# Kernel tuning notes

Measured on AMD Instinct MI355X. Metric: run time of the kernel, lower is better.

## Reference

```python
import jax, jax.numpy as jnp
import numpy as np

# Module/problem constants (match init_kwargs & input_specs)
B, D, H, W = 2, 96, 96, 96
CIN, COUT, K = 16, 32, 3
N = 200000  # number of active (sparse) voxels


def setup_inputs() -> dict:
    key = jax.random.key(0)
    kf, kw, kb = jax.random.split(key, 3)
    # unique valid voxel coordinates -> deterministic scatter semantics
    rng = np.random.default_rng(0)
    lin = rng.choice(B * D * H * W, size=N, replace=False)
    b, z, y, x = np.unravel_index(lin, (B, D, H, W))
    indices = jnp.asarray(np.stack([b, z, y, x], axis=1).astype(np.int32))  # [N,4]
    features = jax.random.normal(kf, (N, CIN), dtype=jnp.float32)
    fan_in = CIN * K ** 3
    conv_w = jax.random.normal(kw, (COUT, CIN, K, K, K), dtype=jnp.float32) / np.sqrt(fan_in)
    conv_b = jax.random.normal(kb, (COUT,), dtype=jnp.float32) * 0.01
    return {"features": features, "indices": indices, "conv_w": conv_w, "conv_b": conv_b}


def reference(features, indices, conv_w, conv_b):
    """DenseFallbackConv3d.forward on a SparseConvTensor, stride=1 path.

    1) scatter sparse features into dense grid [B,CIN,D,H,W]
    2) dense Conv3d (k=3, pad=1, stride=1) + bias
    3) gather per-point output features at the same voxel indices -> [N,COUT]
    """
    b = indices[:, 0]
    z = indices[:, 1]
    y = indices[:, 2]
    x = indices[:, 3]
    # scatter: equivalent of grid[b, :, z, y, x] = features
    grid = jnp.zeros((B, CIN, D, H, W), dtype=features.dtype).at[b, :, z, y, x].set(features)
    out = jax.lax.conv_general_dilated(
        grid, conv_w,
        window_strides=(1, 1, 1),
        padding=((1, 1), (1, 1), (1, 1)),
        dimension_numbers=("NCDHW", "OIDHW", "NCDHW"),
    )
    out = out + conv_b[None, :, None, None, None]
    # gather: out_dense[b, :, z, y, x] for every active voxel -> [N, COUT]
    return out[b, :, z, y, x]
```

## Files before the change

### kernel.cpp

```cpp
#include <hip/hip_runtime.h>

#define BB   2
#define DD   96
#define HH   96
#define WW   96
#define CINC 16
#define COUTC 32
#define KVOL 27
#define GRID_VOX (BB*DD*HH*WW)
#define NW (KVOL*CINC*COUTC)
#define VPT 8
#define CVB (256*VPT)
#define SWP 20

typedef _Float16 half4 __attribute__((ext_vector_type(4)));
typedef _Float16 half8 __attribute__((ext_vector_type(8)));
typedef float    floatx16 __attribute__((ext_vector_type(16)));

__global__ __launch_bounds__(256) void setup_kernel(
        const int* __restrict__ idx, int* __restrict__ g,
        const float* __restrict__ w, _Float16* __restrict__ wH,
        int* __restrict__ counter, int n, int scatter_blocks) {
    if ((int)blockIdx.x < scatter_blocks) {
        int i = blockIdx.x * 256 + threadIdx.x;
        if (i >= n) return;
        int4 v = ((const int4*)idx)[i];
        int lin = ((v.x * DD + v.y) * HH + v.z) * WW + v.w;
        g[lin] = i;
    } else {
        int t = ((int)blockIdx.x - scatter_blocks) * 256 + threadIdx.x;
        if (t == 0) counter[0] = 0;
        if (t >= NW) return;
        int ci = t & (CINC - 1);
        int co = (t >> 4) & (COUTC - 1);
        int kk = t >> 9;
        wH[t] = (_Float16)w[(co * CINC + ci) * KVOL + kk];
    }
}

__global__ __launch_bounds__(256) void compact_kernel(
        const int* __restrict__ idx, const float* __restrict__ feat,
        int* __restrict__ g, _Float16* __restrict__ featH,
        int* __restrict__ pc, int* __restrict__ perm,
        int* __restrict__ counter, int n) {
    __shared__ int s_wsum[4];
    __shared__ int s_wbase[4];
    __shared__ int s_base;
    const int t = threadIdx.x;
    const int lane = t & 63;
    const int wv = t >> 6;
    const int base = blockIdx.x * CVB + t * VPT;

    int4 a0 = ((const int4*)(g + base))[0];
    int4 a1 = ((const int4*)(g + base))[1];
    int vals[VPT] = {a0.x, a0.y, a0.z, a0.w, a1.x, a1.y, a1.z, a1.w};
    int pid[VPT], pck[VPT];
    int cnt = 0;
#pragma unroll
    for (int q = 0; q < VPT; ++q) {
        int p = vals[q];
        bool ok = ((unsigned)p < (unsigned)n);
        int pk = 0;
        if (ok) {
            int4 c = ((const int4*)idx)[p];
            int lin = ((c.x * DD + c.y) * HH + c.z) * WW + c.w;
            ok = (lin == base + q);
            pk = (c.x << 21) | (c.y << 14) | (c.z << 7) | c.w;
        }
        pid[q] = ok ? p : -1;
        pck[q] = pk;
        cnt += ok ? 1 : 0;
    }

    int incl = cnt;
#pragma unroll
    for (int d = 1; d < 64; d <<= 1) {
        int v = __shfl_up(incl, d);
        if (lane >= d) incl += v;
    }
    if (lane == 63) s_wsum[wv] = incl;
    __syncthreads();
    if (t == 0) {
        int t0 = s_wsum[0], t1 = s_wsum[1], t2 = s_wsum[2], t3 = s_wsum[3];
        s_wbase[0] = 0; s_wbase[1] = t0; s_wbase[2] = t0 + t1;
        s_wbase[3] = t0 + t1 + t2;
        s_base = atomicAdd(counter, t0 + t1 + t2 + t3);
    }
    __syncthreads();
    int o = s_base + s_wbase[wv] + incl - cnt;

#pragma unroll
    for (int q = 0; q < VPT; ++q) {
        int tag = n;
        int p = pid[q];
        if (p >= 0) {
            pc[o] = pck[q];
            perm[o] = p;
            const float4* src = (const float4*)(feat + (size_t)p * CINC);
            float4 f0 = src[0], f1 = src[1], f2 = src[2], f3 = src[3];
            half8 h0, h1;
            h0[0]=(_Float16)f0.x; h0[1]=(_Float16)f0.y; h0[2]=(_Float16)f0.z; h0[3]=(_Float16)f0.w;
            h0[4]=(_Float16)f1.x; h0[5]=(_Float16)f1.y; h0[6]=(_Float16)f1.z; h0[7]=(_Float16)f1.w;
            h1[0]=(_Float16)f2.x; h1[1]=(_Float16)f2.y; h1[2]=(_Float16)f2.z; h1[3]=(_Float16)f2.w;
            h1[4]=(_Float16)f3.x; h1[5]=(_Float16)f3.y; h1[6]=(_Float16)f3.z; h1[7]=(_Float16)f3.w;
            half8* dst = (half8*)(featH + (size_t)o * CINC);
            dst[0] = h0; dst[1] = h1;
            tag = o;
            ++o;
        }
        g[base + q] = tag;
    }
    if (blockIdx.x == 0 && t == 0) {
        half8* zr = (half8*)(featH + (size_t)n * CINC);
        half8 hz = {};
        zr[0] = hz; zr[1] = hz;
    }
}

__global__ __launch_bounds__(256, 4) void conv_mfma_kernel(
        const _Float16* __restrict__ featH, const int* __restrict__ pc,
        const int* __restrict__ perm, const _Float16* __restrict__ wH,
        const float* __restrict__ bias, const int* __restrict__ g,
        float* __restrict__ out, int n) {
    __shared__ _Float16 sW[KVOL * 32 * SWP];
    const int lane = threadIdx.x & 63;
    const int wave = threadIdx.x >> 6;
    const int m    = lane & 31;
    const int hf   = lane >> 5;

    for (int u = threadIdx.x; u < KVOL * 64; u += 256) {
        int kk = u >> 6, r = u & 63;
        int co = r >> 1, h = r & 1;
        const half4* src = (const half4*)(wH + kk * (COUTC * CINC) + co * CINC + h * 8);
        half4 v0 = src[0], v1 = src[1];
        _Float16* dst = &sW[kk * 32 * SWP + co * SWP + h * 8];
        *(half4*)dst = v0;
        *(half4*)(dst + 4) = v1;
    }
    __syncthreads();

    const int j0 = (blockIdx.x * 4 + wave) * 32;
    if (j0 >= n) return;
    const int j = j0 + m;

    const int p = pc[j];
    const int x = p & 127, y = (p >> 7) & 127, z = (p >> 14) & 127, b = p >> 21;
    const int base = ((b * DD + z) * HH + y) * WW + x;
    const int pm = perm[j];

    int nid[KVOL];
#pragma unroll
    for (int kk = 0; kk < KVOL; ++kk) {
        const int dz = kk / 9 - 1, dy = (kk / 3) % 3 - 1, dx = kk % 3 - 1;
        int nz = z + dz, ny = y + dy, nx = x + dx;
        bool inb = ((unsigned)nz < DD) & ((unsigned)ny < HH) & ((unsigned)nx < WW);
        int addr = inb ? base + (dz * HH + dy) * WW + dx : 0;
        int v = g[addr];
        nid[kk] = inb ? v : n;
    }

    float bval = bias[m];
    floatx16 acc0, acc1;
#pragma unroll
    for (int i = 0; i < 16; ++i) { acc0[i] = bval; acc1[i] = 0.0f; }

#pragma unroll
    for (int gq = 0; gq < 3; ++gq) {
        half8 av[9];
#pragma unroll
        for (int q = 0; q < 9; ++q)
            av[q] = *(const half8*)(featH + (size_t)nid[gq * 9 + q] * CINC + hf * 8);
#pragma unroll
        for (int q = 0; q < 9; ++q) {
            const int kk = gq * 9 + q;
            const _Float16* bp = &sW[kk * 32 * SWP + m * SWP + hf * 8];
            half4 b0 = *(const half4*)bp;
            half4 b1 = *(const half4*)(bp + 4);
            half8 bf;
            bf[0]=b0[0]; bf[1]=b0[1]; bf[2]=b0[2]; bf[3]=b0[3];
            bf[4]=b1[0]; bf[5]=b1[1]; bf[6]=b1[2]; bf[7]=b1[3];
            if (kk & 1)
                acc1 = __builtin_amdgcn_mfma_f32_32x32x16_f16(av[q], bf, acc1, 0, 0, 0);
            else
                acc0 = __builtin_amdgcn_mfma_f32_32x32x16_f16(av[q], bf, acc0, 0, 0, 0);
        }
    }

#pragma unroll
    for (int i = 0; i < 16; ++i) {
        int r = (i & 3) + 8 * (i >> 2) + 4 * hf;
        int row = __shfl(pm, r);
        out[(size_t)row * COUTC + m] = acc0[i] + acc1[i];
    }
}

extern "C" void kernel_launch(void* const* d_in, const int* in_sizes, int n_in,
                              void* d_out, int out_size, void* d_ws, size_t ws_size,
                              hipStream_t stream) {
    const float* feat  = (const float*)d_in[0];
    const int*   idx   = (const int*)d_in[1];
    const float* convw = (const float*)d_in[2];
    const float* convb = (const float*)d_in[3];
    float* out = (float*)d_out;

    const int n = in_sizes[1] / 4;

    char* ws = (char*)d_ws;
    int*      g       = (int*)ws;
    int*      counter = (int*)(ws + GRID_VOX * 4);
    int*      pc      = (int*)(ws + GRID_VOX * 4 + 256);
    int*      perm    = pc + n;
    _Float16* featH   = (_Float16*)(perm + n);
    _Float16* wH      = featH + (size_t)(n + 1) * CINC;

    const int sb = (n + 255) / 256;
    const int rb = (NW + 255) / 256;
    setup_kernel<<<sb + rb, 256, 0, stream>>>(idx, g, convw, wH, counter, n, sb);
    compact_kernel<<<GRID_VOX / CVB, 256, 0, stream>>>(
        idx, feat, g, featH, pc, perm, counter, n);

    const int waves = (n + 31) / 32;
    conv_mfma_kernel<<<(waves + 3) / 4, 256, 0, stream>>>(
        featH, pc, perm, wH, convb, g, out, n);
}
```

Before: 123.4 us.

## Fuse scatter, compaction and conv into one cooperative persistent kernel

Replaces the three kernel launches with a single cooperative kernel, sized to the occupancy-limited resident block count, that separates the scatter, compaction and MFMA convolution phases with grid-wide barriers. Weights are converted straight into shared memory per block, so the separate half-precision weight buffer is no longer built. The aim is to remove kernel launch gaps and tail effects between stages. In exchange it adds grid-sync cost, grid-stride loops with fewer blocks, and host-side occupancy queries on every call. The conv loop uses n>>5 tiles, which silently drops a trailing partial tile when n is not a multiple of 32 (here n is a multiple of 32).

```diff
diff --git a/kernel.cpp b/kernel.cpp
--- a/kernel.cpp
+++ b/kernel.cpp
@@ -1,4 +1,7 @@
 #include <hip/hip_runtime.h>
+#include <hip/hip_cooperative_groups.h>
+
+namespace cg = cooperative_groups;
 
 #define BB   2
 #define DD   96
@@ -11,11 +14,179 @@
 #define NW (KVOL*CINC*COUTC)
 #define VPT 8
 #define CVB (256*VPT)
+#define NCHUNK (GRID_VOX / CVB)
 #define SWP 20
 
 typedef _Float16 half4 __attribute__((ext_vector_type(4)));
 typedef _Float16 half8 __attribute__((ext_vector_type(8)));
 typedef float    floatx16 __attribute__((ext_vector_type(16)));
+
+__global__ __launch_bounds__(256, 4) void fused_kernel(
+        const float* __restrict__ feat, const int* __restrict__ idx,
+        const float* __restrict__ w, const float* __restrict__ bias,
+        int* __restrict__ g, _Float16* __restrict__ featH,
+        int* __restrict__ pc, int* __restrict__ perm,
+        int* __restrict__ counter, float* __restrict__ out, int n) {
+    __shared__ _Float16 sW[KVOL * 32 * SWP];
+    cg::grid_group grid = cg::this_grid();
+    const int t = threadIdx.x;
+    const int nblk = gridDim.x;
+
+    for (int u = t; u < KVOL * 64; u += 256) {
+        int kk = u >> 6, r = u & 63;
+        int co = r >> 1, h = r & 1;
+        half8 v;
+#pragma unroll
+        for (int q = 0; q < 8; ++q)
+            v[q] = (_Float16)w[(co * CINC + h * 8 + q) * KVOL + kk];
+        _Float16* dst = &sW[kk * 32 * SWP + co * SWP + h * 8];
+        *(half4*)dst = half4{v[0], v[1], v[2], v[3]};
+        *(half4*)(dst + 4) = half4{v[4], v[5], v[6], v[7]};
+    }
+
+    for (int i = blockIdx.x * 256 + t; i < n; i += nblk * 256) {
+        int4 v = ((const int4*)idx)[i];
+        int lin = ((v.x * DD + v.y) * HH + v.z) * WW + v.w;
+        g[lin] = i;
+    }
+    if (blockIdx.x == 0 && t == 0) {
+        counter[0] = 0;
+        half8 hz = {};
+        half8* zr = (half8*)(featH + (size_t)n * CINC);
+        zr[0] = hz; zr[1] = hz;
+    }
+    grid.sync();
+
+    {
+        __shared__ int s_wsum[4];
+        __shared__ int s_wbase[4];
+        __shared__ int s_base;
+        const int lane = t & 63;
+        const int wv = t >> 6;
+        for (int chunk = blockIdx.x; chunk < NCHUNK; chunk += nblk) {
+            const int base = chunk * CVB + t * VPT;
+
+            int4 a0 = ((const int4*)(g + base))[0];
+            int4 a1 = ((const int4*)(g + base))[1];
+            int vals[VPT] = {a0.x, a0.y, a0.z, a0.w, a1.x, a1.y, a1.z, a1.w};
+            int pid[VPT], pck[VPT];
+            int cnt = 0;
+#pragma unroll
+            for (int q = 0; q < VPT; ++q) {
+                int p = vals[q];
+                bool ok = ((unsigned)p < (unsigned)n);
+                int pk = 0;
+                if (ok) {
+                    int4 c = ((const int4*)idx)[p];
+                    int lin = ((c.x * DD + c.y) * HH + c.z) * WW + c.w;
+                    ok = (lin == base + q);
+                    pk = (c.x << 21) | (c.y << 14) | (c.z << 7) | c.w;
+                }
+                pid[q] = ok ? p : -1;
+                pck[q] = pk;
+                cnt += ok ? 1 : 0;
+            }
+
+            int incl = cnt;
+#pragma unroll
+            for (int d = 1; d < 64; d <<= 1) {
+                int v = __shfl_up(incl, d);
+                if (lane >= d) incl += v;
+            }
+            if (lane == 63) s_wsum[wv] = incl;
+            __syncthreads();
+            if (t == 0) {
+                int t0 = s_wsum[0], t1 = s_wsum[1], t2 = s_wsum[2], t3 = s_wsum[3];
+                s_wbase[0] = 0; s_wbase[1] = t0; s_wbase[2] = t0 + t1;
+                s_wbase[3] = t0 + t1 + t2;
+                s_base = atomicAdd(counter, t0 + t1 + t2 + t3);
+            }
+            __syncthreads();
+            int o = s_base + s_wbase[wv] + incl - cnt;
+
+#pragma unroll
+            for (int q = 0; q < VPT; ++q) {
+                int tag = n;
+                int p = pid[q];
+                if (p >= 0) {
+                    pc[o] = pck[q];
+                    perm[o] = p;
+                    const float4* src = (const float4*)(feat + (size_t)p * CINC);
+                    float4 f0 = src[0], f1 = src[1], f2 = src[2], f3 = src[3];
+                    half8 h0, h1;
+                    h0[0]=(_Float16)f0.x; h0[1]=(_Float16)f0.y; h0[2]=(_Float16)f0.z; h0[3]=(_Float16)f0.w;
+                    h0[4]=(_Float16)f1.x; h0[5]=(_Float16)f1.y; h0[6]=(_Float16)f1.z; h0[7]=(_Float16)f1.w;
+                    h1[0]=(_Float16)f2.x; h1[1]=(_Float16)f2.y; h1[2]=(_Float16)f2.z; h1[3]=(_Float16)f2.w;
+                    h1[4]=(_Float16)f3.x; h1[5]=(_Float16)f3.y; h1[6]=(_Float16)f3.z; h1[7]=(_Float16)f3.w;
+                    half8* dst = (half8*)(featH + (size_t)o * CINC);
+                    dst[0] = h0; dst[1] = h1;
+                    tag = o;
+                    ++o;
+                }
+                g[base + q] = tag;
+            }
+        }
+    }
+    grid.sync();
+
+    const int lane = t & 63;
+    const int wave = t >> 6;
+    const int m    = lane & 31;
+    const int hf   = lane >> 5;
+    const float bval = bias[m];
+    const int ntile = n >> 5;
+
+#pragma unroll 1
+    for (int tile = blockIdx.x * 4 + wave; tile < ntile; tile += nblk * 4) {
+        const int j = tile * 32 + m;
+        const int p = pc[j];
+        const int x = p & 127, y = (p >> 7) & 127, z = (p >> 14) & 127, b = p >> 21;
+        const int base = ((b * DD + z) * HH + y) * WW + x;
+        const int pm = perm[j];
+
+        int nid[KVOL];
+#pragma unroll
+        for (int kk = 0; kk < KVOL; ++kk) {
+            const int dz = kk / 9 - 1, dy = (kk / 3) % 3 - 1, dx = kk % 3 - 1;
+            int nz = z + dz, ny = y + dy, nx = x + dx;
+            bool inb = ((unsigned)nz < DD) & ((unsigned)ny < HH) & ((unsigned)nx < WW);
+            int addr = inb ? base + (dz * HH + dy) * WW + dx : 0;
+            int v = g[addr];
+            nid[kk] = inb ? v : n;
+        }
+
+        floatx16 acc0, acc1;
+#pragma unroll
+        for (int i = 0; i < 16; ++i) { acc0[i] = bval; acc1[i] = 0.0f; }
+
+#pragma unroll
+        for (int gq = 0; gq < 3; ++gq) {
+            half8 av[9];
+#pragma unroll
+            for (int q = 0; q < 9; ++q)
+                av[q] = *(const half8*)(featH + (size_t)nid[gq * 9 + q] * CINC + hf * 8);
+#pragma unroll
+            for (int q = 0; q < 9; ++q) {
+                const int kk = gq * 9 + q;
+                const _Float16* bp = &sW[kk * 32 * SWP + m * SWP + hf * 8];
+                half4 b0 = *(const half4*)bp;
+                half4 b1 = *(const half4*)(bp + 4);
+                half8 bf = {b0[0], b0[1], b0[2], b0[3], b1[0], b1[1], b1[2], b1[3]};
+                if (kk & 1)
+                    acc1 = __builtin_amdgcn_mfma_f32_32x32x16_f16(av[q], bf, acc1, 0, 0, 0);
+                else
+                    acc0 = __builtin_amdgcn_mfma_f32_32x32x16_f16(av[q], bf, acc0, 0, 0, 0);
+            }
+        }
+
+#pragma unroll
+        for (int i = 0; i < 16; ++i) {
+            int r = (i & 3) + 8 * (i >> 2) + 4 * hf;
+            int row = __shfl(pm, r);
+            out[(size_t)row * COUTC + m] = acc0[i] + acc1[i];
+        }
+    }
+}
 
 __global__ __launch_bounds__(256) void setup_kernel(
         const int* __restrict__ idx, int* __restrict__ g,
@@ -71,7 +242,6 @@
         pck[q] = pk;
         cnt += ok ? 1 : 0;
     }
-
     int incl = cnt;
 #pragma unroll
     for (int d = 1; d < 64; d <<= 1) {
@@ -88,7 +258,6 @@
     }
     __syncthreads();
     int o = s_base + s_wbase[wv] + incl - cnt;
-
 #pragma unroll
     for (int q = 0; q < VPT; ++q) {
         int tag = n;
@@ -176,9 +345,7 @@
             const _Float16* bp = &sW[kk * 32 * SWP + m * SWP + hf * 8];
             half4 b0 = *(const half4*)bp;
             half4 b1 = *(const half4*)(bp + 4);
-            half8 bf;
-            bf[0]=b0[0]; bf[1]=b0[1]; bf[2]=b0[2]; bf[3]=b0[3];
-            bf[4]=b1[0]; bf[5]=b1[1]; bf[6]=b1[2]; bf[7]=b1[3];
+            half8 bf = {b0[0], b0[1], b0[2], b0[3], b1[0], b1[1], b1[2], b1[3]};
             if (kk & 1)
                 acc1 = __builtin_amdgcn_mfma_f32_32x32x16_f16(av[q], bf, acc1, 0, 0, 0);
             else
@@ -203,7 +370,7 @@
     const float* convb = (const float*)d_in[3];
     float* out = (float*)d_out;
 
-    const int n = in_sizes[1] / 4;
+    int n = in_sizes[1] / 4;
 
     char* ws = (char*)d_ws;
     int*      g       = (int*)ws;
@@ -213,13 +380,31 @@
     _Float16* featH   = (_Float16*)(perm + n);
     _Float16* wH      = featH + (size_t)(n + 1) * CINC;
 
-    const int sb = (n + 255) / 256;
-    const int rb = (NW + 255) / 256;
-    setup_kernel<<<sb + rb, 256, 0, stream>>>(idx, g, convw, wH, counter, n, sb);
-    compact_kernel<<<GRID_VOX / CVB, 256, 0, stream>>>(
-        idx, feat, g, featH, pc, perm, counter, n);
-
-    const int waves = (n + 31) / 32;
-    conv_mfma_kernel<<<(waves + 3) / 4, 256, 0, stream>>>(
-        featH, pc, perm, wH, convb, g, out, n);
+    int dev = 0, ncu = 0, maxb = 0;
+    hipGetDevice(&dev);
+    hipDeviceGetAttribute(&ncu, hipDeviceAttributeMultiprocessorCount, dev);
+    hipError_t oe = hipOccupancyMaxActiveBlocksPerMultiprocessor(
+        &maxb, fused_kernel, 256, 0);
+
+    hipError_t le = hipErrorUnknown;
+    if (oe == hipSuccess && maxb > 0 && ncu > 0) {
+        int nblk = maxb * ncu;
+        if (nblk > 2048) nblk = 2048;
+        void* args[] = { (void*)&feat, (void*)&idx, (void*)&convw, (void*)&convb,
+                         (void*)&g, (void*)&featH, (void*)&pc, (void*)&perm,
+                         (void*)&counter, (void*)&out, (void*)&n };
+        le = hipLaunchCooperativeKernel((void*)fused_kernel,
+                                        dim3(nblk), dim3(256), args, 0, stream);
+    }
+
+    if (le != hipSuccess) {
+        const int sb = (n + 255) / 256;
+        const int rb = (NW + 255) / 256;
+        setup_kernel<<<sb + rb, 256, 0, stream>>>(idx, g, convw, wH, counter, n, sb);
+        compact_kernel<<<GRID_VOX / CVB, 256, 0, stream>>>(
+            idx, feat, g, featH, pc, perm, counter, n);
+        const int waves = (n + 31) / 32;
+        conv_mfma_kernel<<<(waves + 3) / 4, 256, 0, stream>>>(
+            featH, pc, perm, wH, convb, g, out, n);
+    }
 }
```

New measurement: 307.7 us. 149% more time.
